# Kernel tuning notes

Hardware: AMD Instinct MI355X
Metric: run time of the kernel (lower is better)

The kernel has to match this reference:

```python
import jax, jax.numpy as jnp
import numpy as np

NLE_TERM_CO = 80
NUM_CHARS = 256
HID = 128


def setup_inputs() -> dict:
    key = jax.random.key(0)
    ks = jax.random.split(key, 9)
    B = 8192
    message = jax.random.randint(ks[0], (B, NLE_TERM_CO), 0, NUM_CHARS, dtype=jnp.int64)
    # Linear weights stored as (in, out); scaled like torch default init.
    s1 = 1.0 / np.sqrt(NLE_TERM_CO * NUM_CHARS)
    s2 = 1.0 / np.sqrt(HID)
    return {
        "message": message,
        "W1": jax.random.normal(ks[1], (NLE_TERM_CO * NUM_CHARS, HID), jnp.float32) * s1,
        "b1": jax.random.normal(ks[2], (HID,), jnp.float32) * s1,
        "W2": jax.random.normal(ks[3], (HID, HID), jnp.float32) * s2,
        "b2": jax.random.normal(ks[4], (HID,), jnp.float32) * s2,
        "W3": jax.random.normal(ks[5], (HID, HID), jnp.float32) * s2,
        "b3": jax.random.normal(ks[6], (HID,), jnp.float32) * s2,
        "W4": jax.random.normal(ks[7], (HID, HID), jnp.float32) * s2,
        "b4": jax.random.normal(ks[8], (HID,), jnp.float32) * s2,
    }


def reference(message, W1, b1, W2, b2, W3, b3, W4, b4):
    # one_hot(message) @ W1 == gather rows of W1 (viewed [pos, char, hid]) and sum over positions.
    # Exactly the same math (one-hot entries are exact 0.0/1.0 floats).
    W1r = W1.reshape(NLE_TERM_CO, NUM_CHARS, HID)
    pos = jnp.arange(NLE_TERM_CO)  # [80]
    h = W1r[pos, message]          # [B, 80, 128] gather per (position, char)
    h = jax.nn.elu(h.sum(axis=1) + b1)          # [B, 128]
    h = jax.nn.elu(h @ W2 + b2)
    h = jax.nn.elu(h @ W3 + b3)
    h = jax.nn.elu(h @ W4 + b4)
    return h
```

## Files before the change

### kernel.cpp

```cpp
#include <hip/hip_runtime.h>
#include <math.h>

#define HID  128
#define NPOS 80
#define XS   136

typedef float f4 __attribute__((ext_vector_type(4)));
typedef int   i4 __attribute__((ext_vector_type(4)));
typedef unsigned int u32;
typedef __attribute__((ext_vector_type(8))) short bf16x8;
typedef __attribute__((ext_vector_type(4))) float f32x4;

__device__ __forceinline__ float elu(float x) { return x > 0.f ? x : (expf(x) - 1.f); }
__device__ __forceinline__ unsigned short f2bf(float x) {
    u32 u = __float_as_uint(x);
    return (unsigned short)((u + 0x7fffu + ((u >> 16) & 1u)) >> 16);
}
__device__ __forceinline__ float bf2f(unsigned short h) { return __uint_as_float(((u32)h) << 16); }
__device__ __forceinline__ float bflo(u32 v) { return __uint_as_float(v << 16); }
__device__ __forceinline__ float bfhi(u32 v) { return __uint_as_float(v & 0xffff0000u); }

#define W1_BLOCKS 2560
__global__ __launch_bounds__(256) void prep(
    const float* __restrict__ W1, const float* __restrict__ W2,
    const float* __restrict__ W3, const float* __restrict__ W4,
    unsigned short* __restrict__ W1b,
    unsigned short* __restrict__ WtH, unsigned short* __restrict__ WtL)
{
    int b = blockIdx.x;
    if (b < W1_BLOCKS) {
        int i = b * 256 + threadIdx.x;
        f4 f = ((const f4*)W1)[i];
        ushort4 u4;
        u4.x = f2bf(f.x); u4.y = f2bf(f.y); u4.z = f2bf(f.z); u4.w = f2bf(f.w);
        ((ushort4*)W1b)[i] = u4;
    } else {
        int t = (b - W1_BLOCKS) * 256 + threadIdx.x;
        int L = t >> 14;
        int nk = t & 16383;
        int n = nk >> 7, k = nk & 127;
        const float* W = (L == 0) ? W2 : (L == 1) ? W3 : W4;
        float w = W[k * HID + n];
        unsigned short hi = f2bf(w);
        WtH[t] = hi;
        WtL[t] = f2bf(w - bf2f(hi));
    }
}

__global__ __launch_bounds__(256) void gather_k(
    const int* __restrict__ msg, const unsigned short* __restrict__ W1b,
    const float* __restrict__ b1, float* __restrict__ H)
{
    const int tid = threadIdx.x, lane = tid & 63, w = tid >> 6;
    const int row = blockIdx.x * 4 + w;

    __shared__ int smsg[4 * NPOS];
    for (int k = tid; k < 4 * NPOS; k += 256)
        smsg[k] = msg[blockIdx.x * 4 * NPOS + k];
    __syncthreads();

    const int* mrow = &smsg[w * NPOS];
    const int loff = lane << 1;
    float2 bv = *(const float2*)&b1[loff];
    float hx = bv.x, hy = bv.y;

    #pragma unroll 1
    for (int p0 = 0; p0 < NPOS; p0 += 16) {
        i4 ca = *(const i4*)&mrow[p0];
        i4 cb = *(const i4*)&mrow[p0 + 4];
        i4 cc = *(const i4*)&mrow[p0 + 8];
        i4 cd = *(const i4*)&mrow[p0 + 12];
        int c[16] = { ca.x, ca.y, ca.z, ca.w, cb.x, cb.y, cb.z, cb.w,
                      cc.x, cc.y, cc.z, cc.w, cd.x, cd.y, cd.z, cd.w };
        u32 v[16];
        #pragma unroll
        for (int u = 0; u < 16; ++u)
            v[u] = *(const u32*)(W1b + (((p0 + u) << 15) + (c[u] << 7) + loff));
        #pragma unroll
        for (int u = 0; u < 16; ++u) { hx += bflo(v[u]); hy += bfhi(v[u]); }
    }
    *(float2*)&H[row * HID + loff] = make_float2(elu(hx), elu(hy));
}

__global__ __launch_bounds__(256) void dense_k(
    const unsigned short* __restrict__ WtH, const unsigned short* __restrict__ WtL,
    const float* __restrict__ b2, const float* __restrict__ b3,
    const float* __restrict__ b4, float* __restrict__ H)
{
    const int tid = threadIdx.x, lane = tid & 63, w = tid >> 6;
    const int quad = lane >> 4, l15 = lane & 15;
    const int r0 = blockIdx.x * 16;

    __shared__ unsigned short Xh[16 * XS];
    __shared__ unsigned short Xl[16 * XS];

    {
        const int m = tid >> 4, k0 = (tid & 15) << 3;
        f4 a = *(const f4*)&H[(r0 + m) * HID + k0];
        f4 b = *(const f4*)&H[(r0 + m) * HID + k0 + 4];
        float xs[8] = { a.x, a.y, a.z, a.w, b.x, b.y, b.z, b.w };
        unsigned short hs[8], ls[8];
        #pragma unroll
        for (int u = 0; u < 8; ++u) {
            hs[u] = f2bf(xs[u]);
            ls[u] = f2bf(xs[u] - bf2f(hs[u]));
        }
        *(ushort4*)&Xh[m * XS + k0]     = make_ushort4(hs[0], hs[1], hs[2], hs[3]);
        *(ushort4*)&Xh[m * XS + k0 + 4] = make_ushort4(hs[4], hs[5], hs[6], hs[7]);
        *(ushort4*)&Xl[m * XS + k0]     = make_ushort4(ls[0], ls[1], ls[2], ls[3]);
        *(ushort4*)&Xl[m * XS + k0 + 4] = make_ushort4(ls[4], ls[5], ls[6], ls[7]);
    }
    __syncthreads();

    const float* bs[3] = { b2, b3, b4 };

    #pragma unroll 1
    for (int L = 0; L < 3; ++L) {
        bf16x8 Ah[4], Al[4];
        #pragma unroll
        for (int kt = 0; kt < 4; ++kt) {
            const int off = l15 * XS + kt * 32 + quad * 8;
            Ah[kt] = *(const bf16x8*)&Xh[off];
            Al[kt] = *(const bf16x8*)&Xl[off];
        }

        const unsigned short* WH = WtH + L * 16384;
        const unsigned short* WL = WtL + L * 16384;
        f32x4 acc[2] = { {0,0,0,0}, {0,0,0,0} };

        #pragma unroll
        for (int nt = 0; nt < 2; ++nt) {
            const int n = w * 32 + nt * 16 + l15;
            #pragma unroll
            for (int kt = 0; kt < 4; ++kt) {
                const int boff = n * HID + kt * 32 + quad * 8;
                bf16x8 Bh = *(const bf16x8*)&WH[boff];
                bf16x8 Bl = *(const bf16x8*)&WL[boff];
                acc[nt] = __builtin_amdgcn_mfma_f32_16x16x32_bf16(Ah[kt], Bh, acc[nt], 0, 0, 0);
                acc[nt] = __builtin_amdgcn_mfma_f32_16x16x32_bf16(Ah[kt], Bl, acc[nt], 0, 0, 0);
                acc[nt] = __builtin_amdgcn_mfma_f32_16x16x32_bf16(Al[kt], Bh, acc[nt], 0, 0, 0);
            }
        }
        __syncthreads();

        #pragma unroll
        for (int nt = 0; nt < 2; ++nt) {
            const int n = w * 32 + nt * 16 + l15;
            const float bias = bs[L][n];
            #pragma unroll
            for (int r = 0; r < 4; ++r) {
                const int m = quad * 4 + r;
                const float y = elu(acc[nt][r] + bias);
                if (L < 2) {
                    unsigned short hi = f2bf(y);
                    Xh[m * XS + n] = hi;
                    Xl[m * XS + n] = f2bf(y - bf2f(hi));
                } else {
                    H[(r0 + m) * HID + n] = y;
                }
            }
        }
        if (L < 2) __syncthreads();
    }
}

extern "C" void kernel_launch(void* const* d_in, const int* in_sizes, int n_in,
                              void* d_out, int out_size, void* d_ws, size_t ws_size,
                              hipStream_t stream) {
    const int*   msg = (const int*)  d_in[0];
    const float* W1  = (const float*)d_in[1];
    const float* b1  = (const float*)d_in[2];
    const float* W2  = (const float*)d_in[3];
    const float* b2  = (const float*)d_in[4];
    const float* W3  = (const float*)d_in[5];
    const float* b3  = (const float*)d_in[6];
    const float* W4  = (const float*)d_in[7];
    const float* b4  = (const float*)d_in[8];
    float* out = (float*)d_out;

    unsigned short* W1b = (unsigned short*)d_ws;
    unsigned short* WtH = W1b + 2621440;
    unsigned short* WtL = WtH + 49152;

    prep    <<<dim3(W1_BLOCKS + 192), dim3(256), 0, stream>>>(W1, W2, W3, W4, W1b, WtH, WtL);
    gather_k<<<dim3(2048),            dim3(256), 0, stream>>>(msg, W1b, b1, out);
    dense_k <<<dim3(512),             dim3(256), 0, stream>>>(WtH, WtL, b2, b3, b4, out);
}
```

Before: 107.4 us.

## Fuse gather into dense MLP kernel and pre-swizzle MFMA weight fragments

Merges the embedding-gather kernel into the dense MLP kernel. Each block now gathers its 16 rows, with 16 lanes per row loading 16-byte chunks of W1, and writes the ELU result straight to shared-memory bf16 hi/lo buffers. This removes the intermediate fp32 H write/read and one kernel launch. The prep step now stores W2-W4 pre-swizzled in MFMA B-fragment order so each lane reads contiguous 16 bytes, using fewer prep blocks. The trade-off is fewer waves in flight for the gather (512 blocks instead of 2048) and a different per-lane load pattern.

```diff
diff --git a/kernel.cpp b/kernel.cpp
--- a/kernel.cpp
+++ b/kernel.cpp
@@ -6,8 +6,8 @@
 #define XS   136
 
 typedef float f4 __attribute__((ext_vector_type(4)));
-typedef int   i4 __attribute__((ext_vector_type(4)));
 typedef unsigned int u32;
+typedef u32 u32x4 __attribute__((ext_vector_type(4)));
 typedef __attribute__((ext_vector_type(8))) short bf16x8;
 typedef __attribute__((ext_vector_type(4))) float f32x4;
 
@@ -21,6 +21,7 @@
 __device__ __forceinline__ float bfhi(u32 v) { return __uint_as_float(v & 0xffff0000u); }
 
 #define W1_BLOCKS 2560
+#define TR_BLOCKS 24
 __global__ __launch_bounds__(256) void prep(
     const float* __restrict__ W1, const float* __restrict__ W2,
     const float* __restrict__ W3, const float* __restrict__ W4,
@@ -36,84 +37,88 @@
         ((ushort4*)W1b)[i] = u4;
     } else {
         int t = (b - W1_BLOCKS) * 256 + threadIdx.x;
-        int L = t >> 14;
-        int nk = t & 16383;
-        int n = nk >> 7, k = nk & 127;
+        int lane = t & 63;
+        int q = t >> 6;
+        int kt = q & 3;  q >>= 2;
+        int nt = q & 1;  q >>= 1;
+        int w  = q & 3;
+        int L  = q >> 2;
         const float* W = (L == 0) ? W2 : (L == 1) ? W3 : W4;
-        float w = W[k * HID + n];
-        unsigned short hi = f2bf(w);
-        WtH[t] = hi;
-        WtL[t] = f2bf(w - bf2f(hi));
+        const int n    = w * 32 + nt * 16 + (lane & 15);
+        const int quad = lane >> 4;
+        unsigned short hs[8], ls[8];
+        #pragma unroll
+        for (int j = 0; j < 8; ++j) {
+            const int k = kt * 32 + quad * 8 + j;
+            float v = W[k * HID + n];
+            hs[j] = f2bf(v);
+            ls[j] = f2bf(v - bf2f(hs[j]));
+        }
+        *(ushort4*)&WtH[t * 8]     = make_ushort4(hs[0], hs[1], hs[2], hs[3]);
+        *(ushort4*)&WtH[t * 8 + 4] = make_ushort4(hs[4], hs[5], hs[6], hs[7]);
+        *(ushort4*)&WtL[t * 8]     = make_ushort4(ls[0], ls[1], ls[2], ls[3]);
+        *(ushort4*)&WtL[t * 8 + 4] = make_ushort4(ls[4], ls[5], ls[6], ls[7]);
     }
 }
 
-__global__ __launch_bounds__(256) void gather_k(
+__global__ __launch_bounds__(256) void main_k(
     const int* __restrict__ msg, const unsigned short* __restrict__ W1b,
-    const float* __restrict__ b1, float* __restrict__ H)
-{
-    const int tid = threadIdx.x, lane = tid & 63, w = tid >> 6;
-    const int row = blockIdx.x * 4 + w;
-
-    __shared__ int smsg[4 * NPOS];
-    for (int k = tid; k < 4 * NPOS; k += 256)
-        smsg[k] = msg[blockIdx.x * 4 * NPOS + k];
-    __syncthreads();
-
-    const int* mrow = &smsg[w * NPOS];
-    const int loff = lane << 1;
-    float2 bv = *(const float2*)&b1[loff];
-    float hx = bv.x, hy = bv.y;
-
-    #pragma unroll 1
-    for (int p0 = 0; p0 < NPOS; p0 += 16) {
-        i4 ca = *(const i4*)&mrow[p0];
-        i4 cb = *(const i4*)&mrow[p0 + 4];
-        i4 cc = *(const i4*)&mrow[p0 + 8];
-        i4 cd = *(const i4*)&mrow[p0 + 12];
-        int c[16] = { ca.x, ca.y, ca.z, ca.w, cb.x, cb.y, cb.z, cb.w,
-                      cc.x, cc.y, cc.z, cc.w, cd.x, cd.y, cd.z, cd.w };
-        u32 v[16];
-        #pragma unroll
-        for (int u = 0; u < 16; ++u)
-            v[u] = *(const u32*)(W1b + (((p0 + u) << 15) + (c[u] << 7) + loff));
-        #pragma unroll
-        for (int u = 0; u < 16; ++u) { hx += bflo(v[u]); hy += bfhi(v[u]); }
-    }
-    *(float2*)&H[row * HID + loff] = make_float2(elu(hx), elu(hy));
-}
-
-__global__ __launch_bounds__(256) void dense_k(
+    const float* __restrict__ b1,
     const unsigned short* __restrict__ WtH, const unsigned short* __restrict__ WtL,
     const float* __restrict__ b2, const float* __restrict__ b3,
-    const float* __restrict__ b4, float* __restrict__ H)
+    const float* __restrict__ b4, float* __restrict__ out)
 {
     const int tid = threadIdx.x, lane = tid & 63, w = tid >> 6;
     const int quad = lane >> 4, l15 = lane & 15;
-    const int r0 = blockIdx.x * 16;
+    const int m    = w * 4 + quad;
+    const int soff = l15 << 3;
+    const int r0   = blockIdx.x * 16;
 
+    __shared__ int smsg[16 * NPOS];
     __shared__ unsigned short Xh[16 * XS];
     __shared__ unsigned short Xl[16 * XS];
 
+    for (int k = tid; k < 16 * NPOS; k += 256)
+        smsg[k] = msg[r0 * NPOS + k];
+    __syncthreads();
+
+    const int* mrow = &smsg[m * NPOS];
+    f4 acc0 = *(const f4*)&b1[soff];
+    f4 acc1 = *(const f4*)&b1[soff + 4];
+    #pragma unroll 1
+    for (int p0 = 0; p0 < NPOS; p0 += 8) {
+        int c[8];
+        #pragma unroll
+        for (int u = 0; u < 8; ++u) c[u] = mrow[p0 + u];
+        u32x4 v[8];
+        #pragma unroll
+        for (int u = 0; u < 8; ++u)
+            v[u] = *(const u32x4*)&W1b[((p0 + u) << 15) + (c[u] << 7) + soff];
+        #pragma unroll
+        for (int u = 0; u < 8; ++u) {
+            acc0.x += bflo(v[u].x); acc0.y += bfhi(v[u].x);
+            acc0.z += bflo(v[u].y); acc0.w += bfhi(v[u].y);
+            acc1.x += bflo(v[u].z); acc1.y += bfhi(v[u].z);
+            acc1.z += bflo(v[u].w); acc1.w += bfhi(v[u].w);
+        }
+    }
     {
-        const int m = tid >> 4, k0 = (tid & 15) << 3;
-        f4 a = *(const f4*)&H[(r0 + m) * HID + k0];
-        f4 b = *(const f4*)&H[(r0 + m) * HID + k0 + 4];
-        float xs[8] = { a.x, a.y, a.z, a.w, b.x, b.y, b.z, b.w };
+        float xs[8] = { acc0.x, acc0.y, acc0.z, acc0.w, acc1.x, acc1.y, acc1.z, acc1.w };
         unsigned short hs[8], ls[8];
         #pragma unroll
         for (int u = 0; u < 8; ++u) {
-            hs[u] = f2bf(xs[u]);
-            ls[u] = f2bf(xs[u] - bf2f(hs[u]));
+            float y = elu(xs[u]);
+            hs[u] = f2bf(y);
+            ls[u] = f2bf(y - bf2f(hs[u]));
         }
-        *(ushort4*)&Xh[m * XS + k0]     = make_ushort4(hs[0], hs[1], hs[2], hs[3]);
-        *(ushort4*)&Xh[m * XS + k0 + 4] = make_ushort4(hs[4], hs[5], hs[6], hs[7]);
-        *(ushort4*)&Xl[m * XS + k0]     = make_ushort4(ls[0], ls[1], ls[2], ls[3]);
-        *(ushort4*)&Xl[m * XS + k0 + 4] = make_ushort4(ls[4], ls[5], ls[6], ls[7]);
+        *(ushort4*)&Xh[m * XS + soff]     = make_ushort4(hs[0], hs[1], hs[2], hs[3]);
+        *(ushort4*)&Xh[m * XS + soff + 4] = make_ushort4(hs[4], hs[5], hs[6], hs[7]);
+        *(ushort4*)&Xl[m * XS + soff]     = make_ushort4(ls[0], ls[1], ls[2], ls[3]);
+        *(ushort4*)&Xl[m * XS + soff + 4] = make_ushort4(ls[4], ls[5], ls[6], ls[7]);
     }
     __syncthreads();
 
     const float* bs[3] = { b2, b3, b4 };
-
     #pragma unroll 1
     for (int L = 0; L < 3; ++L) {
         bf16x8 Ah[4], Al[4];
@@ -123,17 +128,14 @@
             Ah[kt] = *(const bf16x8*)&Xh[off];
             Al[kt] = *(const bf16x8*)&Xl[off];
         }
-
         const unsigned short* WH = WtH + L * 16384;
         const unsigned short* WL = WtL + L * 16384;
         f32x4 acc[2] = { {0,0,0,0}, {0,0,0,0} };
-
         #pragma unroll
         for (int nt = 0; nt < 2; ++nt) {
-            const int n = w * 32 + nt * 16 + l15;
             #pragma unroll
             for (int kt = 0; kt < 4; ++kt) {
-                const int boff = n * HID + kt * 32 + quad * 8;
+                const int boff = ((((w << 1) + nt) << 2) + kt) * 512 + lane * 8;
                 bf16x8 Bh = *(const bf16x8*)&WH[boff];
                 bf16x8 Bl = *(const bf16x8*)&WL[boff];
                 acc[nt] = __builtin_amdgcn_mfma_f32_16x16x32_bf16(Ah[kt], Bh, acc[nt], 0, 0, 0);
@@ -149,14 +151,14 @@
             const float bias = bs[L][n];
             #pragma unroll
             for (int r = 0; r < 4; ++r) {
-                const int m = quad * 4 + r;
+                const int mm = quad * 4 + r;
                 const float y = elu(acc[nt][r] + bias);
                 if (L < 2) {
                     unsigned short hi = f2bf(y);
-                    Xh[m * XS + n] = hi;
-                    Xl[m * XS + n] = f2bf(y - bf2f(hi));
+                    Xh[mm * XS + n] = hi;
+                    Xl[mm * XS + n] = f2bf(y - bf2f(hi));
                 } else {
-                    H[(r0 + m) * HID + n] = y;
+                    out[(r0 + mm) * HID + n] = y;
                 }
             }
         }
@@ -182,7 +184,7 @@
     unsigned short* WtH = W1b + 2621440;
     unsigned short* WtL = WtH + 49152;
 
-    prep    <<<dim3(W1_BLOCKS + 192), dim3(256), 0, stream>>>(W1, W2, W3, W4, W1b, WtH, WtL);
-    gather_k<<<dim3(2048),            dim3(256), 0, stream>>>(msg, W1b, b1, out);
-    dense_k <<<dim3(512),             dim3(256), 0, stream>>>(WtH, WtL, b2, b3, b4, out);
+    prep  <<<dim3(W1_BLOCKS + TR_BLOCKS), dim3(256), 0, stream>>>(W1, W2, W3, W4, W1b, WtH, WtL);
+    main_k<<<dim3(512),                   dim3(256), 0, stream>>>(msg, W1b, b1, WtH, WtL,
+                                                                  b2, b3, b4, out);
 }
```

Result: faster. 98.07 us (-8.7%).
